# Kernel tuning notes

Measured on AMD Instinct MI355X. Metric: run time of the kernel, lower is better.

The kernel has to match this reference:

```python
import jax, jax.numpy as jnp
import numpy as np

D_MODEL = 1024
H = 16
D_K = D_MODEL // H
B, S = 4, 2048


def setup_inputs() -> dict:
    key = jax.random.key(0)
    ks = jax.random.split(key, 12)
    std = 1.0 / np.sqrt(D_MODEL)
    inp = {
        "q": jax.random.normal(ks[0], (B, S, D_MODEL), dtype=jnp.float32),
        "k": jax.random.normal(ks[1], (B, S, D_MODEL), dtype=jnp.float32),
        "v": jax.random.normal(ks[2], (B, S, D_MODEL), dtype=jnp.float32),
        "mask": jnp.tril(jnp.ones((S, S), dtype=jnp.int32))[None, None],  # [1,1,S,S] causal
        "w_q": jax.random.normal(ks[3], (D_MODEL, D_MODEL), dtype=jnp.float32) * std,
        "b_q": jax.random.normal(ks[4], (D_MODEL,), dtype=jnp.float32) * std,
        "w_k": jax.random.normal(ks[5], (D_MODEL, D_MODEL), dtype=jnp.float32) * std,
        "b_k": jax.random.normal(ks[6], (D_MODEL,), dtype=jnp.float32) * std,
        "w_v": jax.random.normal(ks[7], (D_MODEL, D_MODEL), dtype=jnp.float32) * std,
        "b_v": jax.random.normal(ks[8], (D_MODEL,), dtype=jnp.float32) * std,
        "w_o": jax.random.normal(ks[9], (D_MODEL, D_MODEL), dtype=jnp.float32) * std,
        "b_o": jax.random.normal(ks[10], (D_MODEL,), dtype=jnp.float32) * std,
    }
    return inp


def reference(q, k, v, mask, w_q, b_q, w_k, b_k, w_v, b_v, w_o, b_o):
    b, s, _ = q.shape
    # linear projections (torch Linear: x @ W^T + b)
    query = q @ w_q.T + b_q
    key_ = k @ w_k.T + b_k
    value = v @ w_v.T + b_v
    # [B,S,D] -> [B,H,S,Dk]
    query = query.reshape(b, s, H, D_K).transpose(0, 2, 1, 3)
    key_ = key_.reshape(b, -1, H, D_K).transpose(0, 2, 1, 3)
    value = value.reshape(b, -1, H, D_K).transpose(0, 2, 1, 3)
    scores = jnp.einsum("bhqd,bhkd->bhqk", query, key_) / jnp.sqrt(jnp.float32(D_K))
    scores = jnp.where(mask == 0, jnp.float32(-1e9), scores)
    attn = jax.nn.softmax(scores, axis=-1)
    out = jnp.einsum("bhqk,bhkd->bhqd", attn, value)
    out = out.transpose(0, 2, 1, 3).reshape(b, s, D_MODEL)
    return out @ w_o.T + b_o
```

## Files before the change

### kernel.cpp

```cpp
#include <hip/hip_runtime.h>


typedef _Float16 h8 __attribute__((ext_vector_type(8)));
typedef float f32x4 __attribute__((ext_vector_type(4)));
typedef float f32x16 __attribute__((ext_vector_type(16)));

#define S_LEN 2048
#define DM 1024
#define DK 64

struct H2 { _Float16 h, l; };
__device__ __forceinline__ H2 split2(float v) {
  H2 r; r.h = (_Float16)v; r.l = (_Float16)(v - (float)r.h); return r;
}
__device__ __forceinline__ unsigned int pack2(float a, float b) {
  union { _Float16 h[2]; unsigned int u; } x;
  x.h[0] = (_Float16)a; x.h[1] = (_Float16)b;
  return x.u;
}

#define GLOAD16(gp, lp)                                                        \
  __builtin_amdgcn_global_load_lds(                                            \
      (const __attribute__((address_space(1))) void*)(gp),                     \
      (__attribute__((address_space(3))) void*)(lp), 16, 0, 0)

__global__ __launch_bounds__(256)
void presplit(const float* __restrict__ X, _Float16* __restrict__ Hi,
              _Float16* __restrict__ Lo, int n8) {
  const int i = blockIdx.x * 256 + threadIdx.x;
  if (i >= n8) return;
  const float4 a = ((const float4*)X)[2 * i];
  const float4 b = ((const float4*)X)[2 * i + 1];
  h8 hv, lv;
  H2 s;
  s = split2(a.x); hv[0] = s.h; lv[0] = s.l;
  s = split2(a.y); hv[1] = s.h; lv[1] = s.l;
  s = split2(a.z); hv[2] = s.h; lv[2] = s.l;
  s = split2(a.w); hv[3] = s.h; lv[3] = s.l;
  s = split2(b.x); hv[4] = s.h; lv[4] = s.l;
  s = split2(b.y); hv[5] = s.h; lv[5] = s.l;
  s = split2(b.z); hv[6] = s.h; lv[6] = s.l;
  s = split2(b.w); hv[7] = s.h; lv[7] = s.l;
  *(h8*)&Hi[(size_t)i * 8] = hv;
  *(h8*)&Lo[(size_t)i * 8] = lv;
}

template<int OUT_MODE>
__global__ __launch_bounds__(256)
void gemm_ps(const _Float16* __restrict__ Xhi, const _Float16* __restrict__ Xlo,
             const _Float16* __restrict__ Whi, const _Float16* __restrict__ Wlo,
             const float* __restrict__ bias,
             _Float16* __restrict__ Yhi, _Float16* __restrict__ Ylo,
             float* __restrict__ Yf) {
  __shared__ _Float16 Ah[128 * 32], Al[128 * 32], Bh[128 * 32], Bl[128 * 32];
  const int tid = threadIdx.x;
  const int m0 = blockIdx.x * 128, n0 = blockIdx.y * 128;
  const int wid = tid >> 6, lane = tid & 63;
  const int wm = (wid >> 1) * 64, wn = (wid & 1) * 64;
  const int l15 = lane & 15, lg = lane >> 4;
  const _Float16* gsrc = (wid == 0) ? Xhi : (wid == 1) ? Xlo : (wid == 2) ? Whi : Wlo;
  _Float16* lbase = (wid == 0) ? Ah : (wid == 1) ? Al : (wid == 2) ? Bh : Bl;
  const int rbase = (wid < 2) ? m0 : n0;
  const int rowoff = lane >> 2, coloff = (lane & 3) * 8;
  f32x4 acc[4][4] = {};
  for (int kt = 0; kt < 32; ++kt) {
    const int k0 = kt * 32;
#pragma unroll
    for (int c = 0; c < 8; ++c) {
      GLOAD16(&gsrc[(size_t)(rbase + c * 16 + rowoff) * DM + k0 + coloff],
              &lbase[c * 512]);
    }
    __syncthreads();
    h8 a_h[4], a_l[4], b_h[4], b_l[4];
#pragma unroll
    for (int i = 0; i < 4; ++i) {
      const int ra = (wm + i * 16 + l15) * 32 + lg * 8;
      const int rb = (wn + i * 16 + l15) * 32 + lg * 8;
      a_h[i] = *(const h8*)&Ah[ra];
      a_l[i] = *(const h8*)&Al[ra];
      b_h[i] = *(const h8*)&Bh[rb];
      b_l[i] = *(const h8*)&Bl[rb];
    }
#pragma unroll
    for (int mi = 0; mi < 4; ++mi)
#pragma unroll
      for (int ni = 0; ni < 4; ++ni) {
        acc[mi][ni] = __builtin_amdgcn_mfma_f32_16x16x32_f16(a_h[mi], b_h[ni], acc[mi][ni], 0, 0, 0);
        acc[mi][ni] = __builtin_amdgcn_mfma_f32_16x16x32_f16(a_h[mi], b_l[ni], acc[mi][ni], 0, 0, 0);
        acc[mi][ni] = __builtin_amdgcn_mfma_f32_16x16x32_f16(a_l[mi], b_h[ni], acc[mi][ni], 0, 0, 0);
      }
    __syncthreads();
  }
#pragma unroll
  for (int mi = 0; mi < 4; ++mi)
#pragma unroll
    for (int ni = 0; ni < 4; ++ni)
#pragma unroll
      for (int j = 0; j < 4; ++j) {
        const int rg = m0 + wm + mi * 16 + lg * 4 + j;
        const int cg = n0 + wn + ni * 16 + l15;
        const float v = acc[mi][ni][j] + bias[cg];
        if constexpr (OUT_MODE == 0) {
          H2 s = split2(v);
          Yhi[(size_t)rg * DM + cg] = s.h;
          Ylo[(size_t)rg * DM + cg] = s.l;
        } else {
          Yf[(size_t)rg * DM + cg] = v;
        }
      }
}

__global__ __launch_bounds__(256)
void mha_vtrans(const float* __restrict__ Vp,
                _Float16* __restrict__ Vthi, _Float16* __restrict__ Vtlo) {
  __shared__ float tile[64 * 65];
  const int bh = blockIdx.y, s0 = blockIdx.x * 64;
  const int b = bh >> 4, h = bh & 15;
  const int t = threadIdx.x;
  const int row = t >> 2, cg = (t & 3) * 16;
  const size_t inbase = ((size_t)(b * S_LEN + s0 + row)) * DM + h * DK + cg;
#pragma unroll
  for (int i = 0; i < 4; ++i) {
    const float4 v = *(const float4*)&Vp[inbase + i * 4];
    tile[row * 65 + cg + i * 4 + 0] = v.x;
    tile[row * 65 + cg + i * 4 + 1] = v.y;
    tile[row * 65 + cg + i * 4 + 2] = v.z;
    tile[row * 65 + cg + i * 4 + 3] = v.w;
  }
  __syncthreads();
  const int drow = t >> 2, sg = (t & 3) * 16;
  h8 hv0, hv1, lv0, lv1;
#pragma unroll
  for (int i = 0; i < 8; ++i) {
    H2 a = split2(tile[(sg + i) * 65 + drow]);
    hv0[i] = a.h; lv0[i] = a.l;
    H2 c = split2(tile[(sg + 8 + i) * 65 + drow]);
    hv1[i] = c.h; lv1[i] = c.l;
  }
  const size_t ob = ((size_t)bh * DK + drow) * S_LEN + s0 + sg;
  *(h8*)&Vthi[ob] = hv0;
  *(h8*)&Vthi[ob + 8] = hv1;
  *(h8*)&Vtlo[ob] = lv0;
  *(h8*)&Vtlo[ob + 8] = lv1;
}

__global__ __launch_bounds__(64)
void mha_attn(const _Float16* __restrict__ Qhi, const _Float16* __restrict__ Qlo,
              const _Float16* __restrict__ Khi, const _Float16* __restrict__ Klo,
              const _Float16* __restrict__ Vthi, const _Float16* __restrict__ Vtlo,
              _Float16* __restrict__ Ohi, _Float16* __restrict__ Olo) {
  const int lane = threadIdx.x;
  const int l31 = lane & 31, hi = lane >> 5;
  const int hwid = blockIdx.x + (blockIdx.y << 5);
  const int logical = (hwid & 7) * 256 + (hwid >> 3);
  const int r = logical & 31;
  const int bh = logical >> 5;
  const int fq = 63 - r;
  const int b = bh >> 4, h = bh & 15;
  const size_t rowbase = (size_t)b * S_LEN * DM + h * DK;
  const size_t vbase = (size_t)bh * DK * S_LEN;

  h8 qh_r[4], ql_r[4], qh_f[4], ql_f[4];
#pragma unroll
  for (int ks = 0; ks < 4; ++ks) {
    const size_t offr = rowbase + (size_t)(r * 32 + l31) * DM + ks * 16 + hi * 8;
    const size_t offf = rowbase + (size_t)(fq * 32 + l31) * DM + ks * 16 + hi * 8;
    qh_r[ks] = *(const h8*)&Qhi[offr]; ql_r[ks] = *(const h8*)&Qlo[offr];
    qh_f[ks] = *(const h8*)&Qhi[offf]; ql_f[ks] = *(const h8*)&Qlo[offf];
  }
  f32x16 po0r = {}, po1r = {}, po0f = {}, po1f = {};
  float m_r = -1e30f, l_r = 0.0f, m_f = -1e30f, l_f = 0.0f;

  auto loadK = [&](int t, h8 (&kh)[4], h8 (&kl)[4]) {
    const int c0 = t * 32;
#pragma unroll
    for (int ks = 0; ks < 4; ++ks) {
      const size_t koff = rowbase + (size_t)(c0 + l31) * DM + ks * 16 + hi * 8;
      kh[ks] = *(const h8*)&Khi[koff];
      kl[ks] = *(const h8*)&Klo[koff];
    }
  };

  auto smax_pv = [&](const f32x16& sA, const f32x16& sB, bool diag,
                     float& m, float& l, f32x16& po0, f32x16& po1,
                     const h8 (&vh)[2][2], const h8 (&vl)[2][2]) {
    float p[16];
    float tmax = -3e38f;
#pragma unroll
    for (int rr = 0; rr < 16; ++rr) {
      const int kvr = (rr & 3) + 8 * (rr >> 2) + 4 * hi;
      float sv = (sA[rr] + sB[rr]) * 0.125f;
      if (diag && kvr > l31) sv = -1e30f;
      p[rr] = sv;
      tmax = fmaxf(tmax, sv);
    }
    tmax = fmaxf(tmax, __shfl_xor(tmax, 32, 64));
    const float mnew = fmaxf(m, tmax);
    const float alpha = __expf(m - mnew);
    float tsum = 0.0f;
#pragma unroll
    for (int rr = 0; rr < 16; ++rr) { p[rr] = __expf(p[rr] - mnew); tsum += p[rr]; }
    tsum += __shfl_xor(tsum, 32, 64);
    l = l * alpha + tsum;
    m = mnew;
    po0 = po0 * alpha;
    po1 = po1 * alpha;
    unsigned int pw[8], qw[8];
#pragma unroll
    for (int g = 0; g < 8; ++g) pw[g] = pack2(p[2 * g], p[2 * g + 1]);
#pragma unroll
    for (int g = 0; g < 8; ++g) qw[g] = (unsigned int)__shfl_xor((int)pw[g], 32, 64);
#pragma unroll
    for (int cks = 0; cks < 2; ++cks) {
      union { unsigned int u[4]; h8 v; } bp;
      if (hi == 0) {
        bp.u[0] = pw[4 * cks];     bp.u[1] = pw[4 * cks + 1];
        bp.u[2] = qw[4 * cks];     bp.u[3] = qw[4 * cks + 1];
      } else {
        bp.u[0] = qw[4 * cks + 2]; bp.u[1] = qw[4 * cks + 3];
        bp.u[2] = pw[4 * cks + 2]; bp.u[3] = pw[4 * cks + 3];
      }
      po0 = __builtin_amdgcn_mfma_f32_32x32x16_f16(vh[cks][0], bp.v, po0, 0, 0, 0);
      po0 = __builtin_amdgcn_mfma_f32_32x32x16_f16(vl[cks][0], bp.v, po0, 0, 0, 0);
      po1 = __builtin_amdgcn_mfma_f32_32x32x16_f16(vh[cks][1], bp.v, po1, 0, 0, 0);
      po1 = __builtin_amdgcn_mfma_f32_32x32x16_f16(vl[cks][1], bp.v, po1, 0, 0, 0);
    }
  };

  auto body = [&](int t, const h8 (&kh)[4], const h8 (&kl)[4],
                  h8 (&nkh)[4], h8 (&nkl)[4]) {
    if (t + 1 <= fq) loadK(t + 1, nkh, nkl);
    const int c0 = t * 32;
    h8 vh[2][2], vl[2][2];
#pragma unroll
    for (int cks = 0; cks < 2; ++cks) {
      const size_t voff = vbase + (size_t)l31 * S_LEN + c0 + cks * 16 + hi * 8;
      vh[cks][0] = *(const h8*)&Vthi[voff];
      vl[cks][0] = *(const h8*)&Vtlo[voff];
      vh[cks][1] = *(const h8*)&Vthi[voff + (size_t)32 * S_LEN];
      vl[cks][1] = *(const h8*)&Vtlo[voff + (size_t)32 * S_LEN];
    }
    {
      f32x16 sA = {}, sB = {};
#pragma unroll
      for (int ks = 0; ks < 4; ++ks) {
        sA = __builtin_amdgcn_mfma_f32_32x32x16_f16(kh[ks], qh_f[ks], sA, 0, 0, 0);
        sB = __builtin_amdgcn_mfma_f32_32x32x16_f16(kh[ks], ql_f[ks], sB, 0, 0, 0);
        sB = __builtin_amdgcn_mfma_f32_32x32x16_f16(kl[ks], qh_f[ks], sB, 0, 0, 0);
      }
      smax_pv(sA, sB, t == fq, m_f, l_f, po0f, po1f, vh, vl);
    }
    if (t <= r) {
      f32x16 sA = {}, sB = {};
#pragma unroll
      for (int ks = 0; ks < 4; ++ks) {
        sA = __builtin_amdgcn_mfma_f32_32x32x16_f16(kh[ks], qh_r[ks], sA, 0, 0, 0);
        sB = __builtin_amdgcn_mfma_f32_32x32x16_f16(kh[ks], ql_r[ks], sB, 0, 0, 0);
        sB = __builtin_amdgcn_mfma_f32_32x32x16_f16(kl[ks], qh_r[ks], sB, 0, 0, 0);
      }
      smax_pv(sA, sB, t == r, m_r, l_r, po0r, po1r, vh, vl);
    }
  };

  h8 khA[4], klA[4], khB[4], klB[4];
  loadK(0, khA, klA);
  int t = 0;
  while (true) {
    body(t, khA, klA, khB, klB);
    ++t; if (t > fq) break;
    body(t, khB, klB, khA, klA);
    ++t; if (t > fq) break;
  }

  __shared__ float lds_o[32 * 65];
  auto writeO = [&](int qt, float l, const f32x16& po0, const f32x16& po1) {
    const float invl = 1.0f / l;
#pragma unroll
    for (int rr = 0; rr < 16; ++rr) {
      const int dl = (rr & 3) + 8 * (rr >> 2) + 4 * hi;
      lds_o[l31 * 65 + dl] = po0[rr] * invl;
      lds_o[l31 * 65 + 32 + dl] = po1[rr] * invl;
    }
    __syncthreads();
    const size_t ob = ((size_t)b * S_LEN + qt * 32) * DM + h * DK;
    for (int r2 = 0; r2 < 32; ++r2) {
      H2 s = split2(lds_o[r2 * 65 + lane]);
      Ohi[ob + (size_t)r2 * DM + lane] = s.h;
      Olo[ob + (size_t)r2 * DM + lane] = s.l;
    }
    __syncthreads();
  };
  writeO(fq, l_f, po0f, po1f);
  writeO(r, l_r, po0r, po1r);
}

extern "C" void kernel_launch(void* const* d_in, const int* in_sizes, int n_in,
                              void* d_out, int out_size, void* d_ws, size_t ws_size,
                              hipStream_t stream) {
  const float* q   = (const float*)d_in[0];
  const float* k   = (const float*)d_in[1];
  const float* v   = (const float*)d_in[2];
  const float* w_q = (const float*)d_in[4];
  const float* b_q = (const float*)d_in[5];
  const float* w_k = (const float*)d_in[6];
  const float* b_k = (const float*)d_in[7];
  const float* w_v = (const float*)d_in[8];
  const float* b_v = (const float*)d_in[9];
  const float* w_o = (const float*)d_in[10];
  const float* b_o = (const float*)d_in[11];

  const size_t NIN = (size_t)8192 * 1024;
  const size_t NW  = (size_t)1024 * 1024;
  const size_t SZH = NIN * sizeof(_Float16);
  char* ws = (char*)d_ws;
  _Float16* b1 = (_Float16*)(ws + 0 * SZH);
  _Float16* b2 = (_Float16*)(ws + 2 * SZH);
  _Float16* b3 = (_Float16*)(ws + 4 * SZH);
  char*     b4 = ws + 6 * SZH;

  _Float16* Xhi = b1;            _Float16* Xlo = b1 + NIN;
  _Float16* Qph = b2;            _Float16* Qpl = b2 + NIN;
  _Float16* Kph = b3;            _Float16* Kpl = b3 + NIN;
  float*    Vp  = (float*)b4;
  _Float16* Vth = (_Float16*)b1; _Float16* Vtl = (_Float16*)b1 + NIN;
  _Float16* Oh  = (_Float16*)b4; _Float16* Ol  = (_Float16*)b4 + NIN;
  _Float16* Wdh = (_Float16*)d_out; _Float16* Wdl = (_Float16*)d_out + NW;
  _Float16* Woh = (_Float16*)b2;    _Float16* Wol = (_Float16*)b2 + NW;

  const int NIN8 = (int)(NIN / 8), NW8 = (int)(NW / 8);
  dim3 gg(64, 8);

  presplit<<<4096, 256, 0, stream>>>(q, Xhi, Xlo, NIN8);
  presplit<<<512, 256, 0, stream>>>(w_q, Wdh, Wdl, NW8);
  gemm_ps<0><<<gg, 256, 0, stream>>>(Xhi, Xlo, Wdh, Wdl, b_q, Qph, Qpl, nullptr);
  presplit<<<4096, 256, 0, stream>>>(k, Xhi, Xlo, NIN8);
  presplit<<<512, 256, 0, stream>>>(w_k, Wdh, Wdl, NW8);
  gemm_ps<0><<<gg, 256, 0, stream>>>(Xhi, Xlo, Wdh, Wdl, b_k, Kph, Kpl, nullptr);
  presplit<<<4096, 256, 0, stream>>>(v, Xhi, Xlo, NIN8);
  presplit<<<512, 256, 0, stream>>>(w_v, Wdh, Wdl, NW8);
  gemm_ps<1><<<gg, 256, 0, stream>>>(Xhi, Xlo, Wdh, Wdl, b_v, nullptr, nullptr, Vp);
  mha_vtrans<<<dim3(32, 64), 256, 0, stream>>>(Vp, Vth, Vtl);
  mha_attn<<<dim3(32, 64), 64, 0, stream>>>(Qph, Qpl, Kph, Kpl, Vth, Vtl, Oh, Ol);
  presplit<<<512, 256, 0, stream>>>(w_o, Woh, Wol, NW8);
  gemm_ps<1><<<gg, 256, 0, stream>>>(Oh, Ol, Woh, Wol, b_o, nullptr, nullptr, (float*)d_out);
}
```

Baseline: 641.9 us.

## Double-buffer GEMM LDS tiles, lazy softmax rescale, and MFMA priority hints

The projection GEMM now double-buffers its LDS tiles, issuing the next k-tile's global-to-LDS loads before computing on the current one, which removes one barrier per iteration. The attention softmax skips the running-max rescale of the accumulators when every lane's new max stays within 8 of the old one. s_setprio is raised around the MFMA blocks, and the next K load is moved after the V loads. The extra buffer doubles GEMM LDS use, which may lower occupancy. The lazy rescale lets exponentials grow up to e^8, so precision depends on that bound holding.

```diff
diff --git a/kernel.cpp b/kernel.cpp
--- a/kernel.cpp
+++ b/kernel.cpp
@@ -52,35 +52,42 @@
              const float* __restrict__ bias,
              _Float16* __restrict__ Yhi, _Float16* __restrict__ Ylo,
              float* __restrict__ Yf) {
-  __shared__ _Float16 Ah[128 * 32], Al[128 * 32], Bh[128 * 32], Bl[128 * 32];
+  __shared__ _Float16 lds[2][4][128 * 32];
   const int tid = threadIdx.x;
   const int m0 = blockIdx.x * 128, n0 = blockIdx.y * 128;
   const int wid = tid >> 6, lane = tid & 63;
   const int wm = (wid >> 1) * 64, wn = (wid & 1) * 64;
   const int l15 = lane & 15, lg = lane >> 4;
   const _Float16* gsrc = (wid == 0) ? Xhi : (wid == 1) ? Xlo : (wid == 2) ? Whi : Wlo;
-  _Float16* lbase = (wid == 0) ? Ah : (wid == 1) ? Al : (wid == 2) ? Bh : Bl;
   const int rbase = (wid < 2) ? m0 : n0;
   const int rowoff = lane >> 2, coloff = (lane & 3) * 8;
   f32x4 acc[4][4] = {};
-  for (int kt = 0; kt < 32; ++kt) {
+
+  auto stage = [&](int buf, int kt) {
     const int k0 = kt * 32;
 #pragma unroll
     for (int c = 0; c < 8; ++c) {
       GLOAD16(&gsrc[(size_t)(rbase + c * 16 + rowoff) * DM + k0 + coloff],
-              &lbase[c * 512]);
-    }
-    __syncthreads();
+              &lds[buf][wid][c * 512]);
+    }
+  };
+
+  stage(0, 0);
+  __syncthreads();
+  for (int kt = 0; kt < 32; ++kt) {
+    const int buf = kt & 1;
+    if (kt + 1 < 32) stage(buf ^ 1, kt + 1);
     h8 a_h[4], a_l[4], b_h[4], b_l[4];
 #pragma unroll
     for (int i = 0; i < 4; ++i) {
       const int ra = (wm + i * 16 + l15) * 32 + lg * 8;
       const int rb = (wn + i * 16 + l15) * 32 + lg * 8;
-      a_h[i] = *(const h8*)&Ah[ra];
-      a_l[i] = *(const h8*)&Al[ra];
-      b_h[i] = *(const h8*)&Bh[rb];
-      b_l[i] = *(const h8*)&Bl[rb];
-    }
+      a_h[i] = *(const h8*)&lds[buf][0][ra];
+      a_l[i] = *(const h8*)&lds[buf][1][ra];
+      b_h[i] = *(const h8*)&lds[buf][2][rb];
+      b_l[i] = *(const h8*)&lds[buf][3][rb];
+    }
+    __builtin_amdgcn_s_setprio(1);
 #pragma unroll
     for (int mi = 0; mi < 4; ++mi)
 #pragma unroll
@@ -89,6 +96,7 @@
         acc[mi][ni] = __builtin_amdgcn_mfma_f32_16x16x32_f16(a_h[mi], b_l[ni], acc[mi][ni], 0, 0, 0);
         acc[mi][ni] = __builtin_amdgcn_mfma_f32_16x16x32_f16(a_l[mi], b_h[ni], acc[mi][ni], 0, 0, 0);
       }
+    __builtin_amdgcn_s_setprio(0);
     __syncthreads();
   }
 #pragma unroll
@@ -195,21 +203,25 @@
       tmax = fmaxf(tmax, sv);
     }
     tmax = fmaxf(tmax, __shfl_xor(tmax, 32, 64));
-    const float mnew = fmaxf(m, tmax);
-    const float alpha = __expf(m - mnew);
+    if (!__all(tmax <= m + 8.0f)) {
+      const float mnew = fmaxf(m, tmax);
+      const float alpha = __expf(m - mnew);
+      l *= alpha;
+      po0 = po0 * alpha;
+      po1 = po1 * alpha;
+      m = mnew;
+    }
     float tsum = 0.0f;
 #pragma unroll
-    for (int rr = 0; rr < 16; ++rr) { p[rr] = __expf(p[rr] - mnew); tsum += p[rr]; }
+    for (int rr = 0; rr < 16; ++rr) { p[rr] = __expf(p[rr] - m); tsum += p[rr]; }
     tsum += __shfl_xor(tsum, 32, 64);
-    l = l * alpha + tsum;
-    m = mnew;
-    po0 = po0 * alpha;
-    po1 = po1 * alpha;
+    l += tsum;
     unsigned int pw[8], qw[8];
 #pragma unroll
     for (int g = 0; g < 8; ++g) pw[g] = pack2(p[2 * g], p[2 * g + 1]);
 #pragma unroll
     for (int g = 0; g < 8; ++g) qw[g] = (unsigned int)__shfl_xor((int)pw[g], 32, 64);
+    __builtin_amdgcn_s_setprio(1);
 #pragma unroll
     for (int cks = 0; cks < 2; ++cks) {
       union { unsigned int u[4]; h8 v; } bp;
@@ -225,11 +237,11 @@
       po1 = __builtin_amdgcn_mfma_f32_32x32x16_f16(vh[cks][1], bp.v, po1, 0, 0, 0);
       po1 = __builtin_amdgcn_mfma_f32_32x32x16_f16(vl[cks][1], bp.v, po1, 0, 0, 0);
     }
+    __builtin_amdgcn_s_setprio(0);
   };
 
   auto body = [&](int t, const h8 (&kh)[4], const h8 (&kl)[4],
                   h8 (&nkh)[4], h8 (&nkl)[4]) {
-    if (t + 1 <= fq) loadK(t + 1, nkh, nkl);
     const int c0 = t * 32;
     h8 vh[2][2], vl[2][2];
 #pragma unroll
@@ -240,24 +252,29 @@
       vh[cks][1] = *(const h8*)&Vthi[voff + (size_t)32 * S_LEN];
       vl[cks][1] = *(const h8*)&Vtlo[voff + (size_t)32 * S_LEN];
     }
+    if (t + 1 <= fq) loadK(t + 1, nkh, nkl);
     {
       f32x16 sA = {}, sB = {};
+      __builtin_amdgcn_s_setprio(1);
 #pragma unroll
       for (int ks = 0; ks < 4; ++ks) {
         sA = __builtin_amdgcn_mfma_f32_32x32x16_f16(kh[ks], qh_f[ks], sA, 0, 0, 0);
         sB = __builtin_amdgcn_mfma_f32_32x32x16_f16(kh[ks], ql_f[ks], sB, 0, 0, 0);
         sB = __builtin_amdgcn_mfma_f32_32x32x16_f16(kl[ks], qh_f[ks], sB, 0, 0, 0);
       }
+      __builtin_amdgcn_s_setprio(0);
       smax_pv(sA, sB, t == fq, m_f, l_f, po0f, po1f, vh, vl);
     }
     if (t <= r) {
       f32x16 sA = {}, sB = {};
+      __builtin_amdgcn_s_setprio(1);
 #pragma unroll
       for (int ks = 0; ks < 4; ++ks) {
         sA = __builtin_amdgcn_mfma_f32_32x32x16_f16(kh[ks], qh_r[ks], sA, 0, 0, 0);
         sB = __builtin_amdgcn_mfma_f32_32x32x16_f16(kh[ks], ql_r[ks], sB, 0, 0, 0);
         sB = __builtin_amdgcn_mfma_f32_32x32x16_f16(kl[ks], qh_r[ks], sB, 0, 0, 0);
       }
+      __builtin_amdgcn_s_setprio(0);
       smax_pv(sA, sB, t == r, m_r, l_r, po0r, po1r, vh, vl);
     }
   };
```

After: 636.4 us. No clear change (-0.9%).
